# Kernel optimization log

Measured on AMD Instinct MI355X. Metric: run time of the kernel, lower is better.

## Reference

```python
import jax, jax.numpy as jnp
import numpy as np
from jax import lax

B, C, H, W = 16, 512, 32, 32
CQ = C // 8  # 64
EPS = 1e-5
NEG_SLOPE = 0.2


def _conv1x1(x, Wm, b):
    # x: [B,C,H,W], Wm: [O,C] (1x1 conv kernel squeezed), b: [O]
    return jnp.einsum('oc,bchw->bohw', Wm, x) + b[None, :, None, None]


def _calc_mean_std(feat):
    b, c = feat.shape[:2]
    v = feat.reshape(b, c, -1)
    mean = v.mean(axis=2)[:, :, None, None]
    var = v.var(axis=2, ddof=1) + EPS  # torch .var is unbiased
    std = jnp.sqrt(var)[:, :, None, None]
    return mean, std


def setup_inputs() -> dict:
    key = jax.random.key(0)
    ks = jax.random.split(key, 8)
    s = 0.02
    return {
        'inp': jax.random.normal(ks[0], (B, C, H, W), jnp.float32),
        'x': jax.random.normal(ks[1], (B, C, H, W), jnp.float32),
        'y': jax.random.normal(ks[2], (B, C, H, W), jnp.float32),
        'Wq': jax.random.normal(ks[3], (CQ, C), jnp.float32) * s,
        'bq': jnp.zeros((CQ,), jnp.float32),
        'Wk': jax.random.normal(ks[4], (CQ, C), jnp.float32) * s,
        'bk': jnp.zeros((CQ,), jnp.float32),
        'Wv': jax.random.normal(ks[5], (C, C), jnp.float32) * s,
        'bv': jnp.zeros((C,), jnp.float32),
        'Wc': jax.random.normal(ks[6], (C, 2 * C, 3, 3), jnp.float32) * s,
        'bc': jnp.zeros((C,), jnp.float32),
        'alpha': jnp.ones((1,), jnp.float32),
        'beta': jnp.ones((1,), jnp.float32),
    }


def reference(inp, x, y, Wq, bq, Wk, bk, Wv, bv, Wc, bc, alpha, beta):
    b, c, h, w = x.shape
    n = h * w
    t = float(CQ) ** 0.5  # default temperature sqrt(c_in//8)

    # --- identity-row attention: query from x, key from y ---
    pq = _conv1x1(x, Wq, bq).reshape(b, CQ, n)   # [b,cq,n]
    pk = _conv1x1(y, Wk, bk).reshape(b, CQ, n)
    pv = _conv1x1(x, Wv, bv).reshape(b, c, n)    # [b,c,n]
    attn_iden = jax.nn.softmax(jnp.einsum('bcn,bcm->bnm', pq, pk) / t, axis=-1)

    # --- pose-row attention: query from y, key from x ---
    pq_p = _conv1x1(y, Wq, bq).reshape(b, CQ, n)
    pk_p = _conv1x1(x, Wk, bk).reshape(b, CQ, n)
    attn_pose = jax.nn.softmax(jnp.einsum('bcn,bcm->bnm', pq_p, pk_p) / t, axis=-1)

    # x_update = bmm(value, attn_iden^T): out[c,m] = sum_n pv[c,n]*attn[m,n]
    x_update = jnp.einsum('bcn,bmn->bcm', pv, attn_iden).reshape(b, c, h, w)
    x_update = (1.0 - beta) * x + beta * x_update

    # --- AdaIN: normalize inp, re-affine with x stats ---
    t_mean, t_std = _calc_mean_std(x)
    i_mean, i_std = _calc_mean_std(inp)
    adained = (inp - i_mean) / i_std * t_std + t_mean

    # reverse attention combine with (1 - attn_pose)
    rev = jnp.einsum('bcn,bmn->bcm', adained.reshape(b, c, n), 1.0 - attn_pose)
    rev = rev.reshape(b, c, h, w)
    rev = (1.0 - alpha) * rev + alpha * adained

    # --- conv_comp: 3x3 conv (2C -> C), same padding, LeakyReLU(0.2) ---
    cat = jnp.concatenate([x_update, rev], axis=1)  # [b,2c,h,w]
    out = lax.conv_general_dilated(
        cat, Wc, window_strides=(1, 1), padding='SAME',
        dimension_numbers=('NCHW', 'OIHW', 'NCHW'))
    out = out + bc[None, :, None, None]
    out = jnp.where(out >= 0, out, NEG_SLOPE * out)
    return out
```

## Files before the change

kernel.cpp:

```cpp
#include <hip/hip_runtime.h>

typedef unsigned short u16;
typedef unsigned int u32;

using bf16x8 = __attribute__((ext_vector_type(8))) __bf16;
using f32x4  = __attribute__((ext_vector_type(4))) float;
using u16x4  = __attribute__((ext_vector_type(4))) unsigned short;

__device__ __forceinline__ f32x4 MFMA(bf16x8 a, bf16x8 b, f32x4 c) {
    return __builtin_amdgcn_mfma_f32_16x16x32_bf16(a, b, c, 0, 0, 0);
}

__device__ __forceinline__ u16 f2bf(float f) {
    u32 u = __builtin_bit_cast(u32, f);
    u = (u + 0x7FFFu + ((u >> 16) & 1u)) >> 16;
    return (u16)u;
}
__device__ __forceinline__ float bf2f(u16 h) {
    return __builtin_bit_cast(float, (u32)h << 16);
}

typedef const __attribute__((address_space(1))) unsigned int* gp_t;
typedef __attribute__((address_space(3))) unsigned int* lp_t;

__device__ __forceinline__ void gload16(const void* g, void* l) {
    __builtin_amdgcn_global_load_lds((gp_t)g, (lp_t)l, 16, 0, 0);
}

#define NPADR  1156

static constexpr size_t OFF_XT   = 0;
static constexpr size_t OFF_YT   = OFF_XT  + (size_t)16*1024*512*2;
static constexpr size_t OFF_PJX  = OFF_YT  + (size_t)16*1024*512*2;
static constexpr size_t OFF_PJY  = OFF_PJX + (size_t)16*1024*128*2;
static constexpr size_t OFF_PV   = OFF_PJY + (size_t)16*1024*128*2;
static constexpr size_t OFF_AD   = OFF_PV  + (size_t)16*512*1024*2;
static constexpr size_t OFF_ATTN = OFF_AD  + (size_t)16*512*1024*2;
static constexpr size_t OFF_ATT2 = OFF_ATTN+ (size_t)16*1024*1024*2;
static constexpr size_t OFF_CATT = OFF_ATT2+ (size_t)16*1024*1024*2;
static constexpr size_t OFF_WQK  = OFF_CATT+ (size_t)16*1156*1024*2;
static constexpr size_t OFF_WV   = OFF_WQK + (size_t)128*512*2;
static constexpr size_t OFF_WT   = OFF_WV  + (size_t)512*512*2;
static constexpr size_t OFF_SA   = OFF_WT  + (size_t)9*512*1024*2;
static constexpr size_t OFF_OA   = OFF_SA  + (size_t)16*512*4;
static constexpr size_t OFF_TM   = OFF_OA  + (size_t)16*512*4;

__global__ __launch_bounds__(256) void k_prep_w(const float* __restrict__ Wq,
                                                const float* __restrict__ Wk,
                                                const float* __restrict__ Wv,
                                                u16* __restrict__ wqk, u16* __restrict__ wv) {
    int i = blockIdx.x * 256 + threadIdx.x;
    if (i < 128 * 512) {
        float v = (i < 64 * 512) ? Wq[i] : Wk[i - 64 * 512];
        wqk[i] = f2bf(v);
    }
    if (i < 512 * 512) wv[i] = f2bf(Wv[i]);
}

__global__ __launch_bounds__(256) void k_prep_wt(const float* __restrict__ Wc, u16* __restrict__ wt) {
    int e = blockIdx.x * 256 + threadIdx.x;
    const float* src = Wc + (size_t)e * 9;
#pragma unroll
    for (int tap = 0; tap < 9; tap++) wt[(size_t)tap * 524288 + e] = f2bf(src[tap]);
}

__global__ __launch_bounds__(256) void k_border(u16* __restrict__ catT) {
    int cell = blockIdx.x, b = blockIdx.y;
    int row, col;
    if (cell < 34)       { row = 0;  col = cell; }
    else if (cell < 68)  { row = 33; col = cell - 34; }
    else if (cell < 100) { row = cell - 68 + 1;  col = 0; }
    else                 { row = cell - 100 + 1; col = 33; }
    u16* dst = catT + ((size_t)b * NPADR + row * 34 + col) * 1024;
    u16x4 z = {0, 0, 0, 0};
    ((u16x4*)dst)[threadIdx.x] = z;
}

__global__ __launch_bounds__(256) void k_stats(const float* __restrict__ x, const float* __restrict__ inp,
                                               u16* __restrict__ ad, float* __restrict__ tmA) {
    int row = blockIdx.x;
    int t = threadIdx.x;
    const float4* xr = (const float4*)(x + (size_t)row * 1024);
    const float4* ir = (const float4*)(inp + (size_t)row * 1024);
    float4 a = xr[t], c = ir[t];
    float s1 = a.x + a.y + a.z + a.w;
    float s2 = a.x * a.x + a.y * a.y + a.z * a.z + a.w * a.w;
    float p1 = c.x + c.y + c.z + c.w;
    float p2 = c.x * c.x + c.y * c.y + c.z * c.z + c.w * c.w;
#pragma unroll
    for (int m = 32; m; m >>= 1) {
        s1 += __shfl_xor(s1, m); s2 += __shfl_xor(s2, m);
        p1 += __shfl_xor(p1, m); p2 += __shfl_xor(p2, m);
    }
    __shared__ float red[4][4];
    __shared__ float bcast[2];
    int wv = t >> 6;
    if ((t & 63) == 0) { red[wv][0] = s1; red[wv][1] = s2; red[wv][2] = p1; red[wv][3] = p2; }
    __syncthreads();
    if (t == 0) {
        s1 = red[0][0] + red[1][0] + red[2][0] + red[3][0];
        s2 = red[0][1] + red[1][1] + red[2][1] + red[3][1];
        p1 = red[0][2] + red[1][2] + red[2][2] + red[3][2];
        p2 = red[0][3] + red[1][3] + red[2][3] + red[3][3];
        float tm = s1 * (1.0f / 1024.0f);
        float ts = sqrtf((s2 - 1024.0f * tm * tm) * (1.0f / 1023.0f) + 1e-5f);
        float im = p1 * (1.0f / 1024.0f);
        float is = sqrtf((p2 - 1024.0f * im * im) * (1.0f / 1023.0f) + 1e-5f);
        float sc = ts / is;
        bcast[0] = sc; bcast[1] = tm - im * sc;
        tmA[row] = tm;
    }
    __syncthreads();
    float sc = bcast[0], of = bcast[1];
    u16x4 r;
    r[0] = f2bf(c.x * sc + of); r[1] = f2bf(c.y * sc + of);
    r[2] = f2bf(c.z * sc + of); r[3] = f2bf(c.w * sc + of);
    ((u16x4*)(ad + (size_t)row * 1024))[t] = r;
}

__global__ __launch_bounds__(256) void k_transpose(const float* __restrict__ x, const float* __restrict__ y,
                                                   u16* __restrict__ xT, u16* __restrict__ yT) {
    __shared__ float tile[64][65];
    int b = blockIdx.y;
    int ct = blockIdx.x >> 4;
    int nt = blockIdx.x & 15;
    const float* src = blockIdx.z ? y : x;
    u16* dst = blockIdx.z ? yT : xT;
    int c0 = ct * 64, n0 = nt * 64;
    int ln = threadIdx.x & 63, wv = threadIdx.x >> 6;
#pragma unroll
    for (int i = 0; i < 16; i++) {
        int cl = wv + i * 4;
        tile[cl][ln] = src[((size_t)(b * 512 + c0 + cl)) * 1024 + n0 + ln];
    }
    __syncthreads();
#pragma unroll
    for (int i = 0; i < 16; i++) {
        int nl = wv + i * 4;
        dst[((size_t)(b * 1024 + n0 + nl)) * 512 + c0 + ln] = f2bf(tile[ln][nl]);
    }
}

template <int KTOT, int LDA, int LDB>
__device__ __forceinline__ void gemm128(const u16* __restrict__ Aorig, const u16* __restrict__ Borig,
                                        f32x4 (&acc)[4][4]) {
    __shared__ __align__(16) u16 lds[32768];
    constexpr int NT = KTOT / 32;
    const int tid = threadIdx.x;
    const int l = tid & 63, w = tid >> 6;
    const int lr = l & 15, lg = l >> 4;
    const int moff = (w >> 1) * 64, coff = (w & 1) * 64;
    char* ldsb = (char*)lds;
    auto stage = [&](const u16* orig, int ldx, int bufByte) {
#pragma unroll
        for (int it = 0; it < 2; it++) {
            int slot = it * 256 + tid;
            gload16(orig + (size_t)(slot & 127) * ldx + (slot >> 7) * 8,
                    ldsb + bufByte + it * 4096 + w * 1024);
        }
    };
    auto stageT = [&](int t, int s) {
        stage(Aorig + t * 32, LDA, s * 8192);
        stage(Borig + t * 32, LDB, 32768 + s * 8192);
    };
    stageT(0, 0);
    stageT(1, 1);
    stageT(2, 2);
#pragma unroll 1
    for (int q = 0; q < NT; q++) {
        int qq = q + 3; if (qq >= NT) qq -= NT;
        stageT(qq, (q + 3) & 3);
        asm volatile("s_waitcnt vmcnt(12)" ::: "memory");
        __builtin_amdgcn_s_barrier();
        const char* A = ldsb + (q & 3) * 8192;
        const char* B = ldsb + 32768 + (q & 3) * 8192;
        bf16x8 af[4], bb[4];
#pragma unroll
        for (int i = 0; i < 4; i++) af[i] = *(const bf16x8*)(A + lg * 2048 + (moff + 16 * i + lr) * 16);
#pragma unroll
        for (int i = 0; i < 4; i++) bb[i] = *(const bf16x8*)(B + lg * 2048 + (coff + 16 * i + lr) * 16);
        __builtin_amdgcn_s_setprio(1);
#pragma unroll
        for (int ri = 0; ri < 4; ri++)
#pragma unroll
            for (int ci = 0; ci < 4; ci++) acc[ri][ci] = MFMA(af[ri], bb[ci], acc[ri][ci]);
        __builtin_amdgcn_s_setprio(0);
        __builtin_amdgcn_s_barrier();
    }
    asm volatile("s_waitcnt vmcnt(0)" ::: "memory");
}

__global__ __launch_bounds__(256) void k_proj(const u16* __restrict__ xT, const u16* __restrict__ yT,
                                              const u16* __restrict__ wqk, const float* __restrict__ bq,
                                              const float* __restrict__ bk, u16* __restrict__ pjx,
                                              u16* __restrict__ pjy) {
    int b = blockIdx.y;
    const u16* S = blockIdx.z ? yT : xT;
    u16* D = blockIdx.z ? pjy : pjx;
    int nb = blockIdx.x * 128;
    f32x4 acc[4][4];
#pragma unroll
    for (int i = 0; i < 4; i++)
#pragma unroll
        for (int j = 0; j < 4; j++) acc[i][j] = f32x4{0.f, 0.f, 0.f, 0.f};
    gemm128<512, 512, 512>(S + ((size_t)b * 1024 + nb) * 512, wqk, acc);
    int l = threadIdx.x & 63, w = threadIdx.x >> 6;
    int lr = l & 15, lg = l >> 4;
    int moff = (w >> 1) * 64, coff = (w & 1) * 64;
#pragma unroll
    for (int ri = 0; ri < 4; ri++) {
#pragma unroll
        for (int r = 0; r < 4; r++) {
            int n = nb + moff + 16 * ri + 4 * lg + r;
#pragma unroll
            for (int ci = 0; ci < 4; ci++) {
                int cq = coff + 16 * ci + lr;
                float bias = (cq < 64) ? bq[cq] : bk[cq - 64];
                D[((size_t)b * 1024 + n) * 128 + cq] = f2bf(acc[ri][ci][r] + bias);
            }
        }
    }
}

__global__ __launch_bounds__(256) void k_pv(const u16* __restrict__ xT, const u16* __restrict__ wv,
                                            const float* __restrict__ bv, u16* __restrict__ pv) {
    int b = blockIdx.z;
    int mb = blockIdx.y * 128;
    int nb = blockIdx.x * 128;
    f32x4 acc[4][4];
#pragma unroll
    for (int i = 0; i < 4; i++)
#pragma unroll
        for (int j = 0; j < 4; j++) acc[i][j] = f32x4{0.f, 0.f, 0.f, 0.f};
    gemm128<512, 512, 512>(wv + (size_t)mb * 512, xT + ((size_t)b * 1024 + nb) * 512, acc);
    int l = threadIdx.x & 63, w = threadIdx.x >> 6;
    int lr = l & 15, lg = l >> 4;
    int moff = (w >> 1) * 64, coff = (w & 1) * 64;
#pragma unroll
    for (int ri = 0; ri < 4; ri++) {
#pragma unroll
        for (int r = 0; r < 4; r++) {
            int co = mb + moff + 16 * ri + 4 * lg + r;
            float bias = bv[co];
#pragma unroll
            for (int ci = 0; ci < 4; ci++) {
                int n = nb + coff + 16 * ci + lr;
                pv[((size_t)b * 512 + co) * 1024 + n] = f2bf(acc[ri][ci][r] + bias);
            }
        }
    }
}

__global__ __launch_bounds__(256) void k_score(const u16* __restrict__ pjx, const u16* __restrict__ pjy,
                                               u16* __restrict__ attnA, u16* __restrict__ attnB) {
    const u16* qT = blockIdx.y ? pjy : pjx;
    const u16* kT = blockIdx.y ? pjx : pjy;
    u16* attn = blockIdx.y ? attnB : attnA;
    int g = blockIdx.x * 4 + (threadIdx.x >> 6);
    int b = g >> 6, rb = g & 63;
    int l = threadIdx.x & 63, lr = l & 15, lg = l >> 4;
    int mb = rb * 16;
    const u16* qbase = qT + ((size_t)b * 1024 + mb + lr) * 128 + lg * 8;
    bf16x8 a0 = *(const bf16x8*)(qbase);
    bf16x8 a1 = *(const bf16x8*)(qbase + 32);
    const u16* kbase = kT + ((size_t)b * 1024 + lr) * 128 + 64 + lg * 8;
    f32x4 zero = {0.f, 0.f, 0.f, 0.f};
    float ref[4], srun[4];
    {
        bf16x8 b0 = *(const bf16x8*)(kbase);
        bf16x8 b1 = *(const bf16x8*)(kbase + 32);
        f32x4 acc = zero;
        acc = MFMA(a0, b0, acc);
        acc = MFMA(a1, b1, acc);
#pragma unroll
        for (int r = 0; r < 4; r++) { ref[r] = acc[r] * 0.125f; srun[r] = 1.0f; }
    }
    for (int cf = 1; cf < 64; cf++) {
        bf16x8 b0 = *(const bf16x8*)(kbase + (size_t)cf * 16 * 128);
        bf16x8 b1 = *(const bf16x8*)(kbase + (size_t)cf * 16 * 128 + 32);
        f32x4 acc = zero;
        acc = MFMA(a0, b0, acc);
        acc = MFMA(a1, b1, acc);
#pragma unroll
        for (int r = 0; r < 4; r++) srun[r] += __expf(acc[r] * 0.125f - ref[r]);
    }
    float inv[4];
#pragma unroll
    for (int r = 0; r < 4; r++) {
        float R = __shfl(ref[r], l & 0x30);
        srun[r] *= __expf(ref[r] - R);
#pragma unroll
        for (int m = 1; m < 16; m <<= 1) srun[r] += __shfl_xor(srun[r], m);
        ref[r] = R;
        inv[r] = 1.0f / srun[r];
    }
    for (int cf = 0; cf < 64; cf++) {
        bf16x8 b0 = *(const bf16x8*)(kbase + (size_t)cf * 16 * 128);
        bf16x8 b1 = *(const bf16x8*)(kbase + (size_t)cf * 16 * 128 + 32);
        f32x4 acc = zero;
        acc = MFMA(a0, b0, acc);
        acc = MFMA(a1, b1, acc);
#pragma unroll
        for (int r = 0; r < 4; r++) {
            float v = __expf(acc[r] * 0.125f - ref[r]) * inv[r];
            attn[((size_t)b * 1024 + mb + 4 * lg + r) * 1024 + cf * 16 + lr] = f2bf(v);
        }
    }
}

__global__ __launch_bounds__(512, 2) void k_value(const u16* __restrict__ attnA, const u16* __restrict__ attnB,
                                                  const u16* __restrict__ pv, const u16* __restrict__ ad,
                                                  const u16* __restrict__ xT, const float* __restrict__ tmA,
                                                  const float* __restrict__ alpha, const float* __restrict__ beta,
                                                  u16* __restrict__ catT) {
    extern __shared__ __align__(16) char dyn[];
    const int id = blockIdx.x;
    const int xcd = id & 7, j = id >> 3;
    const int z = xcd + 8 * (j & 3);
    const int tile = j >> 2;
    const int mbt = tile & 3, cbt = tile >> 2;
    const int b = z & 15, var = z >> 4;
    const u16* Aorig = (var ? attnB : attnA) + ((size_t)b * 1024 + mbt * 256) * 1024;
    const u16* Borig = (var ? ad : pv) + ((size_t)b * 512 + cbt * 256) * 1024;

    const int tid = threadIdx.x;
    const int l = tid & 63, w = tid >> 6;
    const int lr = l & 15, lg = l >> 4;
    const int ow = w >> 1, pw = w & 1;

    auto stageT = [&](int t, int s) {
        char* base = dyn + s * 32768;
#pragma unroll
        for (int it = 0; it < 2; it++) {
            int idx = it * 512 + tid;
            int row = idx & 255, g = idx >> 8;
            gload16(Aorig + (size_t)row * 1024 + t * 32 + g * 8, base + g * 4096 + row * 16);
        }
#pragma unroll
        for (int it = 0; it < 2; it++) {
            int idx = it * 512 + tid;
            int row = idx & 255, g = idx >> 8;
            gload16(Borig + (size_t)row * 1024 + t * 32 + g * 8, base + 16384 + g * 4096 + row * 16);
        }
    };

    f32x4 acc[4][8];
#pragma unroll
    for (int i = 0; i < 4; i++)
#pragma unroll
        for (int jj = 0; jj < 8; jj++) acc[i][jj] = f32x4{0.f, 0.f, 0.f, 0.f};

    stageT(0, 0);
    stageT(1, 1);
#pragma unroll 1
    for (int q = 0; q < 32; q++) {
        int qq = q + 2; if (qq >= 32) qq -= 32;
        stageT(qq, (q + 2) % 3);
        asm volatile("s_waitcnt vmcnt(8)" ::: "memory");
        __builtin_amdgcn_s_barrier();
        const char* A = dyn + (q % 3) * 32768;
        const char* B = A + 16384;
        bf16x8 af[4], bb[8];
#pragma unroll
        for (int i = 0; i < 4; i++) af[i] = *(const bf16x8*)(A + lg * 4096 + (ow * 64 + 16 * i + lr) * 16);
#pragma unroll
        for (int i = 0; i < 8; i++) bb[i] = *(const bf16x8*)(B + lg * 4096 + (pw * 128 + 16 * i + lr) * 16);
        __builtin_amdgcn_s_setprio(1);
#pragma unroll
        for (int ri = 0; ri < 4; ri++)
#pragma unroll
            for (int ci = 0; ci < 8; ci++) acc[ri][ci] = MFMA(af[ri], bb[ci], acc[ri][ci]);
        __builtin_amdgcn_s_setprio(0);
        __builtin_amdgcn_s_barrier();
    }
    asm volatile("s_waitcnt vmcnt(0)" ::: "memory");

    float sc = var ? alpha[0] : beta[0];
#pragma unroll
    for (int ri = 0; ri < 4; ri++) {
#pragma unroll
        for (int r = 0; r < 4; r++) {
            int m = mbt * 256 + ow * 64 + 16 * ri + 4 * lg + r;
            int pidx = ((m >> 5) + 1) * 34 + (m & 31) + 1;
#pragma unroll
            for (int ci = 0; ci < 8; ci++) {
                int c = cbt * 256 + pw * 128 + 16 * ci + lr;
                float av = acc[ri][ci][r];
                float res;
                if (var == 0) {
                    float xv = bf2f(xT[((size_t)b * 1024 + m) * 512 + c]);
                    res = (1.f - sc) * xv + sc * av;
                } else {
                    float tm = tmA[b * 512 + c];
                    float adv = bf2f(ad[((size_t)b * 512 + c) * 1024 + m]);
                    res = (1.f - sc) * (1024.f * tm - av) + sc * adv;
                }
                catT[((size_t)b * NPADR + pidx) * 1024 + (var ? 512 : 0) + c] = f2bf(res);
            }
        }
    }
}

__global__ __launch_bounds__(512, 2) void k_conv(const u16* __restrict__ wt, const u16* __restrict__ catT,
                                                 const float* __restrict__ bc, float* __restrict__ out) {
    extern __shared__ __align__(16) char dyn[];
    const int id = blockIdx.x;
    const int xcd = id & 7, j = id >> 3;
    const int obt = j & 3;
    const int pbb = xcd + 8 * (j >> 2);
    const int pbt = pbb & 3, b = pbb >> 2;

    const int tid = threadIdx.x;
    const int l = tid & 63, w = tid >> 6;
    const int lr = l & 15, lg = l >> 4;
    const int ob = obt * 128;
    const int pb = pbt * 256;
    const int r0 = pbt * 8;
    const int ow = w >> 2, pw = w & 3;
    const u16* catB = catT + (size_t)b * NPADR * 1024 + (size_t)r0 * 34 * 1024;

    auto stageA = [&](int tap, int ck, int slot) {
        char* base = dyn + slot * 8192;
        int row = tid & 127, g = tid >> 7;
        gload16(wt + ((size_t)tap * 512 + ob + row) * 1024 + ck + g * 8,
                base + g * 2048 + row * 16);
    };
    auto stageB = [&](int ck, int sel) {
        char* base = dyn + 32768 + sel * 24576;
#pragma unroll
        for (int it = 0; it < 3; it++) {
            int idx = it * 512 + tid;
            int g = idx / 384;
            int row = idx - g * 384;
            gload16(catB + (size_t)row * 1024 + ck + g * 8,
                    base + g * 6144 + row * 16);
        }
    };

    int aoff[4], rbase[4];
#pragma unroll
    for (int i = 0; i < 4; i++) {
        aoff[i] = lg * 2048 + (ow * 64 + 16 * i + lr) * 16;
        int p = pw * 64 + 16 * i + lr;
        rbase[i] = ((p >> 5) + 1) * 34 + (p & 31) + 1;
    }

    f32x4 acc[4][4];
#pragma unroll
    for (int i = 0; i < 4; i++)
#pragma unroll
        for (int jj = 0; jj < 4; jj++) acc[i][jj] = f32x4{0.f, 0.f, 0.f, 0.f};

    stageA(0, 0, 0);
    stageB(0, 0);
    stageA(1, 0, 1);
    int phase = 0;
#pragma unroll 1
    for (int ckI = 0; ckI < 32; ckI++) {
#pragma unroll
        for (int tap = 0; tap < 9; tap++, phase++) {
            {
                int t2 = tap + 2;
                int c2 = ckI + (t2 >= 9);
                if (t2 >= 9) t2 -= 9;
                if (c2 >= 32) c2 = 0;
                stageA(t2, c2 * 32, (phase + 2) & 3);
            }
            if (tap == 5) {
                int cn = ckI + 1;
                stageB((cn >= 32 ? 0 : cn) * 32, cn & 1);
            }
            if (tap >= 5 && tap <= 7) asm volatile("s_waitcnt vmcnt(5)" ::: "memory");
            else                      asm volatile("s_waitcnt vmcnt(2)" ::: "memory");
            __builtin_amdgcn_s_barrier();
            const char* A = dyn + (phase & 3) * 8192;
            const char* B = dyn + 32768 + (ckI & 1) * 24576;
            const int drow = (tap / 3 - 1) * 34 + (tap % 3 - 1);
            bf16x8 af[4], bb[4];
#pragma unroll
            for (int i = 0; i < 4; i++) af[i] = *(const bf16x8*)(A + aoff[i]);
#pragma unroll
            for (int i = 0; i < 4; i++) bb[i] = *(const bf16x8*)(B + lg * 6144 + (rbase[i] + drow) * 16);
            __builtin_amdgcn_s_setprio(1);
#pragma unroll
            for (int ri = 0; ri < 4; ri++)
#pragma unroll
                for (int ci = 0; ci < 4; ci++) acc[ri][ci] = MFMA(af[ri], bb[ci], acc[ri][ci]);
            __builtin_amdgcn_s_setprio(0);
        }
    }
    asm volatile("s_waitcnt vmcnt(0)" ::: "memory");
#pragma unroll
    for (int ri = 0; ri < 4; ri++) {
#pragma unroll
        for (int r = 0; r < 4; r++) {
            int o = ob + ow * 64 + 16 * ri + 4 * lg + r;
            float bias = bc[o];
#pragma unroll
            for (int ci = 0; ci < 4; ci++) {
                int p = pb + pw * 64 + 16 * ci + lr;
                float v = acc[ri][ci][r] + bias;
                v = (v >= 0.f) ? v : 0.2f * v;
                out[((size_t)b * 512 + o) * 1024 + p] = v;
            }
        }
    }
}

extern "C" void kernel_launch(void* const* d_in, const int* in_sizes, int n_in,
                              void* d_out, int out_size, void* d_ws, size_t ws_size,
                              hipStream_t stream) {
    (void)in_sizes; (void)n_in; (void)out_size; (void)ws_size;
    const float* inp = (const float*)d_in[0];
    const float* x   = (const float*)d_in[1];
    const float* y   = (const float*)d_in[2];
    const float* Wq  = (const float*)d_in[3];
    const float* bq  = (const float*)d_in[4];
    const float* Wk  = (const float*)d_in[5];
    const float* bk  = (const float*)d_in[6];
    const float* Wv  = (const float*)d_in[7];
    const float* bv  = (const float*)d_in[8];
    const float* Wc  = (const float*)d_in[9];
    const float* bc  = (const float*)d_in[10];
    const float* alpha = (const float*)d_in[11];
    const float* beta  = (const float*)d_in[12];
    float* out = (float*)d_out;

    char* ws = (char*)d_ws;
    u16* xT   = (u16*)(ws + OFF_XT);
    u16* yT   = (u16*)(ws + OFF_YT);
    u16* pjx  = (u16*)(ws + OFF_PJX);
    u16* pjy  = (u16*)(ws + OFF_PJY);
    u16* pv   = (u16*)(ws + OFF_PV);
    u16* ad   = (u16*)(ws + OFF_AD);
    u16* attnA = (u16*)(ws + OFF_ATTN);
    u16* attnB = (u16*)(ws + OFF_ATT2);
    u16* catT = (u16*)(ws + OFF_CATT);
    u16* wqk  = (u16*)(ws + OFF_WQK);
    u16* wv   = (u16*)(ws + OFF_WV);
    u16* wt   = (u16*)(ws + OFF_WT);
    float* tmA = (float*)(ws + OFF_TM);

    hipFuncSetAttribute((const void*)k_conv,  hipFuncAttributeMaxDynamicSharedMemorySize, 81920);
    hipFuncSetAttribute((const void*)k_value, hipFuncAttributeMaxDynamicSharedMemorySize, 98304);

    k_prep_w<<<1024, 256, 0, stream>>>(Wq, Wk, Wv, wqk, wv);
    k_prep_wt<<<2048, 256, 0, stream>>>(Wc, wt);
    k_border<<<dim3(132, 16), 256, 0, stream>>>(catT);
    k_stats<<<8192, 256, 0, stream>>>(x, inp, ad, tmA);
    k_transpose<<<dim3(128, 16, 2), 256, 0, stream>>>(x, y, xT, yT);
    k_proj<<<dim3(8, 16, 2), 256, 0, stream>>>(xT, yT, wqk, bq, bk, pjx, pjy);
    k_pv<<<dim3(8, 4, 16), 256, 0, stream>>>(xT, wv, bv, pv);
    k_score<<<dim3(256, 2), 256, 0, stream>>>(pjx, pjy, attnA, attnB);
    k_value<<<256, 512, 98304, stream>>>(attnA, attnB, pv, ad, xT, tmA, alpha, beta, catT);
    k_conv<<<256, 512, 81920, stream>>>(wt, catT, bc, out);
}
```

Before: 378.5 us.

## Single-pass unnormalized softmax scores; deepen conv pipeline to two taps per barrier

k_score now does one pass over keys instead of two. It takes a row reference from the first tile, stores unnormalized exponentials, and writes per-row inverse sums that k_value applies in its epilogue. This removes a full MFMA and exp sweep over the key matrix. k_conv is restructured to process two taps per barrier, with 9 weight staging slots and a larger LDS footprint. It is limited to one block per CU, trading occupancy for fewer barriers and deeper prefetch. Using the first-tile value as the reference instead of the true max risks larger bf16 exponentials, and the deferred normalization must be consistent with how k_value forms the reverse-attention term.

Measured after the change: 357.3 us. 1.06x faster.

```diff
diff --git a/kernel.cpp b/kernel.cpp
--- a/kernel.cpp
+++ b/kernel.cpp
@@ -42,8 +42,8 @@
 static constexpr size_t OFF_WV   = OFF_WQK + (size_t)128*512*2;
 static constexpr size_t OFF_WT   = OFF_WV  + (size_t)512*512*2;
 static constexpr size_t OFF_SA   = OFF_WT  + (size_t)9*512*1024*2;
-static constexpr size_t OFF_OA   = OFF_SA  + (size_t)16*512*4;
-static constexpr size_t OFF_TM   = OFF_OA  + (size_t)16*512*4;
+static constexpr size_t OFF_TM   = OFF_SA  + (size_t)2*16*512*4;
+static constexpr size_t OFF_SB   = OFF_TM  + (size_t)16*512*4;
 
 __global__ __launch_bounds__(256) void k_prep_w(const float* __restrict__ Wq,
                                                 const float* __restrict__ Wk,
@@ -252,10 +252,12 @@
 }
 
 __global__ __launch_bounds__(256) void k_score(const u16* __restrict__ pjx, const u16* __restrict__ pjy,
-                                               u16* __restrict__ attnA, u16* __restrict__ attnB) {
+                                               u16* __restrict__ attnA, u16* __restrict__ attnB,
+                                               float* __restrict__ srA, float* __restrict__ srB) {
     const u16* qT = blockIdx.y ? pjy : pjx;
     const u16* kT = blockIdx.y ? pjx : pjy;
     u16* attn = blockIdx.y ? attnB : attnA;
+    float* sr = blockIdx.y ? srB : srA;
     int g = blockIdx.x * 4 + (threadIdx.x >> 6);
     int b = g >> 6, rb = g & 63;
     int l = threadIdx.x & 63, lr = l & 15, lg = l >> 4;
@@ -273,26 +275,10 @@
         acc = MFMA(a0, b0, acc);
         acc = MFMA(a1, b1, acc);
 #pragma unroll
-        for (int r = 0; r < 4; r++) { ref[r] = acc[r] * 0.125f; srun[r] = 1.0f; }
-    }
-    for (int cf = 1; cf < 64; cf++) {
-        bf16x8 b0 = *(const bf16x8*)(kbase + (size_t)cf * 16 * 128);
-        bf16x8 b1 = *(const bf16x8*)(kbase + (size_t)cf * 16 * 128 + 32);
-        f32x4 acc = zero;
-        acc = MFMA(a0, b0, acc);
-        acc = MFMA(a1, b1, acc);
-#pragma unroll
-        for (int r = 0; r < 4; r++) srun[r] += __expf(acc[r] * 0.125f - ref[r]);
-    }
-    float inv[4];
-#pragma unroll
-    for (int r = 0; r < 4; r++) {
-        float R = __shfl(ref[r], l & 0x30);
-        srun[r] *= __expf(ref[r] - R);
-#pragma unroll
-        for (int m = 1; m < 16; m <<= 1) srun[r] += __shfl_xor(srun[r], m);
-        ref[r] = R;
-        inv[r] = 1.0f / srun[r];
+        for (int r = 0; r < 4; r++) {
+            ref[r] = __shfl(acc[r] * 0.125f, l & 0x30);
+            srun[r] = 0.f;
+        }
     }
     for (int cf = 0; cf < 64; cf++) {
         bf16x8 b0 = *(const bf16x8*)(kbase + (size_t)cf * 16 * 128);
@@ -302,15 +288,26 @@
         acc = MFMA(a1, b1, acc);
 #pragma unroll
         for (int r = 0; r < 4; r++) {
-            float v = __expf(acc[r] * 0.125f - ref[r]) * inv[r];
-            attn[((size_t)b * 1024 + mb + 4 * lg + r) * 1024 + cf * 16 + lr] = f2bf(v);
-        }
+            float e = __expf(acc[r] * 0.125f - ref[r]);
+            srun[r] += e;
+            attn[((size_t)b * 1024 + mb + 4 * lg + r) * 1024 + cf * 16 + lr] = f2bf(e);
+        }
+    }
+#pragma unroll
+    for (int r = 0; r < 4; r++) {
+#pragma unroll
+        for (int m = 1; m < 16; m <<= 1) srun[r] += __shfl_xor(srun[r], m);
+    }
+    if (lr == 0) {
+#pragma unroll
+        for (int r = 0; r < 4; r++) sr[b * 1024 + mb + 4 * lg + r] = 1.0f / srun[r];
     }
 }
 
 __global__ __launch_bounds__(512, 2) void k_value(const u16* __restrict__ attnA, const u16* __restrict__ attnB,
                                                   const u16* __restrict__ pv, const u16* __restrict__ ad,
                                                   const u16* __restrict__ xT, const float* __restrict__ tmA,
+                                                  const float* __restrict__ srA, const float* __restrict__ srB,
                                                   const float* __restrict__ alpha, const float* __restrict__ beta,
                                                   u16* __restrict__ catT) {
     extern __shared__ __align__(16) char dyn[];
@@ -322,6 +319,7 @@
     const int b = z & 15, var = z >> 4;
     const u16* Aorig = (var ? attnB : attnA) + ((size_t)b * 1024 + mbt * 256) * 1024;
     const u16* Borig = (var ? ad : pv) + ((size_t)b * 512 + cbt * 256) * 1024;
+    const float* sr = (var ? srB : srA) + b * 1024;
 
     const int tid = threadIdx.x;
     const int l = tid & 63, w = tid >> 6;
@@ -382,10 +380,11 @@
         for (int r = 0; r < 4; r++) {
             int m = mbt * 256 + ow * 64 + 16 * ri + 4 * lg + r;
             int pidx = ((m >> 5) + 1) * 34 + (m & 31) + 1;
+            float ivm = sr[m];
 #pragma unroll
             for (int ci = 0; ci < 8; ci++) {
                 int c = cbt * 256 + pw * 128 + 16 * ci + lr;
-                float av = acc[ri][ci][r];
+                float av = acc[ri][ci][r] * ivm;
                 float res;
                 if (var == 0) {
                     float xv = bf2f(xT[((size_t)b * 1024 + m) * 512 + c]);
@@ -401,7 +400,7 @@
     }
 }
 
-__global__ __launch_bounds__(512, 2) void k_conv(const u16* __restrict__ wt, const u16* __restrict__ catT,
+__global__ __launch_bounds__(512, 1) void k_conv(const u16* __restrict__ wt, const u16* __restrict__ catT,
                                                  const float* __restrict__ bc, float* __restrict__ out) {
     extern __shared__ __align__(16) char dyn[];
     const int id = blockIdx.x;
@@ -419,20 +418,20 @@
     const int ow = w >> 2, pw = w & 3;
     const u16* catB = catT + (size_t)b * NPADR * 1024 + (size_t)r0 * 34 * 1024;
 
-    auto stageA = [&](int tap, int ck, int slot) {
+    auto stageA = [&](int tap, int ckoff, int slot) {
         char* base = dyn + slot * 8192;
         int row = tid & 127, g = tid >> 7;
-        gload16(wt + ((size_t)tap * 512 + ob + row) * 1024 + ck + g * 8,
+        gload16(wt + ((size_t)tap * 512 + ob + row) * 1024 + ckoff + g * 8,
                 base + g * 2048 + row * 16);
     };
-    auto stageB = [&](int ck, int sel) {
-        char* base = dyn + 32768 + sel * 24576;
+    auto stageB = [&](int ckoff, int sel) {
+        char* base = dyn + 73728 + sel * 24576;
 #pragma unroll
         for (int it = 0; it < 3; it++) {
             int idx = it * 512 + tid;
             int g = idx / 384;
             int row = idx - g * 384;
-            gload16(catB + (size_t)row * 1024 + ck + g * 8,
+            gload16(catB + (size_t)row * 1024 + ckoff + g * 8,
                     base + g * 6144 + row * 16);
         }
     };
@@ -452,40 +451,63 @@
         for (int jj = 0; jj < 4; jj++) acc[i][jj] = f32x4{0.f, 0.f, 0.f, 0.f};
 
     stageA(0, 0, 0);
+    stageA(1, 0, 1);
     stageB(0, 0);
-    stageA(1, 0, 1);
-    int phase = 0;
+    stageA(2, 0, 2);
+    stageA(3, 0, 3);
+
+    static constexpr int TAPS0[9] = {4, 6, 8, 1, 3, 5, 7, 0, 2};
+    static constexpr int CKD0[9]  = {0, 0, 0, 1, 1, 1, 1, 2, 2};
+    static constexpr int TAPS1[9] = {5, 7, 0, 2, 4, 6, 8, 1, 3};
+    static constexpr int CKD1[9]  = {0, 0, 1, 1, 1, 1, 1, 2, 2};
+    static constexpr int DROW0[9] = {-35, -33, 0, 33, 35, -34, -1, 1, 34};
+    static constexpr int DROW1[9] = {-34, -1, 1, 34, -35, -33, 0, 33, 35};
+    static constexpr int SLC0[9] = {0, 2, 4, 6, 8, 1, 3, 5, 7};
+    static constexpr int SLC1[9] = {1, 3, 5, 7, 0, 2, 4, 6, 8};
+    static constexpr int SLS0[9] = {4, 6, 8, 1, 3, 5, 7, 0, 2};
+    static constexpr int SLS1[9] = {5, 7, 0, 2, 4, 6, 8, 1, 3};
+
 #pragma unroll 1
-    for (int ckI = 0; ckI < 32; ckI++) {
-#pragma unroll
-        for (int tap = 0; tap < 9; tap++, phase++) {
+    for (int cc = 0; cc < 16; cc++) {
+#pragma unroll
+        for (int u = 0; u < 9; u++) {
             {
-                int t2 = tap + 2;
-                int c2 = ckI + (t2 >= 9);
-                if (t2 >= 9) t2 -= 9;
-                if (c2 >= 32) c2 = 0;
-                stageA(t2, c2 * 32, (phase + 2) & 3);
-            }
-            if (tap == 5) {
-                int cn = ckI + 1;
-                stageB((cn >= 32 ? 0 : cn) * 32, cn & 1);
-            }
-            if (tap >= 5 && tap <= 7) asm volatile("s_waitcnt vmcnt(5)" ::: "memory");
-            else                      asm volatile("s_waitcnt vmcnt(2)" ::: "memory");
+                int ck = 2 * cc + CKD0[u];
+                stageA(TAPS0[u], (ck >= 32 ? 0 : ck) * 32, SLS0[u]);
+            }
+            {
+                int ck = 2 * cc + CKD1[u];
+                stageA(TAPS1[u], (ck >= 32 ? 0 : ck) * 32, SLS1[u]);
+            }
+            if (u == 2) { int cn = 2 * cc + 1; stageB(cn * 32, 1); }
+            if (u == 6) { int cn = 2 * cc + 2; stageB((cn >= 32 ? 0 : cn) * 32, 0); }
+            if (u == 2 || u == 3 || u >= 6) asm volatile("s_waitcnt vmcnt(7)" ::: "memory");
+            else                            asm volatile("s_waitcnt vmcnt(4)" ::: "memory");
             __builtin_amdgcn_s_barrier();
-            const char* A = dyn + (phase & 3) * 8192;
-            const char* B = dyn + 32768 + (ckI & 1) * 24576;
-            const int drow = (tap / 3 - 1) * 34 + (tap % 3 - 1);
-            bf16x8 af[4], bb[4];
-#pragma unroll
-            for (int i = 0; i < 4; i++) af[i] = *(const bf16x8*)(A + aoff[i]);
-#pragma unroll
-            for (int i = 0; i < 4; i++) bb[i] = *(const bf16x8*)(B + lg * 6144 + (rbase[i] + drow) * 16);
+            const char* A0 = dyn + SLC0[u] * 8192;
+            const char* A1 = dyn + SLC1[u] * 8192;
+            const char* B0 = dyn + 73728 + ((u >= 5) ? 24576 : 0);
+            const char* B1 = dyn + 73728 + ((u >= 4) ? 24576 : 0);
+            bf16x8 af0[4], bb0[4], af1[4], bb1[4];
+#pragma unroll
+            for (int i = 0; i < 4; i++) {
+                af0[i] = *(const bf16x8*)(A0 + aoff[i]);
+                bb0[i] = *(const bf16x8*)(B0 + lg * 6144 + (rbase[i] + DROW0[u]) * 16);
+            }
+#pragma unroll
+            for (int i = 0; i < 4; i++) {
+                af1[i] = *(const bf16x8*)(A1 + aoff[i]);
+                bb1[i] = *(const bf16x8*)(B1 + lg * 6144 + (rbase[i] + DROW1[u]) * 16);
+            }
             __builtin_amdgcn_s_setprio(1);
 #pragma unroll
             for (int ri = 0; ri < 4; ri++)
 #pragma unroll
-                for (int ci = 0; ci < 4; ci++) acc[ri][ci] = MFMA(af[ri], bb[ci], acc[ri][ci]);
+                for (int ci = 0; ci < 4; ci++) acc[ri][ci] = MFMA(af0[ri], bb0[ci], acc[ri][ci]);
+#pragma unroll
+            for (int ri = 0; ri < 4; ri++)
+#pragma unroll
+                for (int ci = 0; ci < 4; ci++) acc[ri][ci] = MFMA(af1[ri], bb1[ci], acc[ri][ci]);
             __builtin_amdgcn_s_setprio(0);
         }
     }
@@ -539,9 +561,11 @@
     u16* wqk  = (u16*)(ws + OFF_WQK);
     u16* wv   = (u16*)(ws + OFF_WV);
     u16* wt   = (u16*)(ws + OFF_WT);
+    float* srA = (float*)(ws + OFF_SA);
     float* tmA = (float*)(ws + OFF_TM);
-
-    hipFuncSetAttribute((const void*)k_conv,  hipFuncAttributeMaxDynamicSharedMemorySize, 81920);
+    float* srB = (float*)(ws + OFF_SB);
+
+    hipFuncSetAttribute((const void*)k_conv,  hipFuncAttributeMaxDynamicSharedMemorySize, 122880);
     hipFuncSetAttribute((const void*)k_value, hipFuncAttributeMaxDynamicSharedMemorySize, 98304);
 
     k_prep_w<<<1024, 256, 0, stream>>>(Wq, Wk, Wv, wqk, wv);
@@ -551,7 +575,7 @@
     k_transpose<<<dim3(128, 16, 2), 256, 0, stream>>>(x, y, xT, yT);
     k_proj<<<dim3(8, 16, 2), 256, 0, stream>>>(xT, yT, wqk, bq, bk, pjx, pjy);
     k_pv<<<dim3(8, 4, 16), 256, 0, stream>>>(xT, wv, bv, pv);
-    k_score<<<dim3(256, 2), 256, 0, stream>>>(pjx, pjy, attnA, attnB);
-    k_value<<<256, 512, 98304, stream>>>(attnA, attnB, pv, ad, xT, tmA, alpha, beta, catT);
-    k_conv<<<256, 512, 81920, stream>>>(wt, catT, bc, out);
-}
+    k_score<<<dim3(256, 2), 256, 0, stream>>>(pjx, pjy, attnA, attnB, srA, srB);
+    k_value<<<256, 512, 98304, stream>>>(attnA, attnB, pv, ad, xT, tmA, srA, srB, alpha, beta, catT);
+    k_conv<<<256, 512, 122880, stream>>>(wt, catT, bc, out);
+}
```
